# Performance work log

Hardware: AMD Instinct MI355X
Metric: run time of the kernel (lower is better)

The kernel has to match this reference:

```python
import jax, jax.numpy as jnp
import numpy as np

N = 50000
IN_DIM = 128
HID = 16
HEADS = 8
NUM_CLASSES = 16
NEG_SLOPE = 0.2


def _glorot(key, shape):
    fan_in, fan_out = shape[0], shape[-1]
    lim = float(np.sqrt(6.0 / (fan_in + fan_out)))
    return jax.random.uniform(key, shape, jnp.float32, -lim, lim)


def setup_inputs() -> dict:
    key = jax.random.key(0)
    ks = jax.random.split(key, 12)
    x = jax.random.normal(ks[0], (N, IN_DIM), jnp.float32)
    edge_index = jax.random.randint(ks[1], (2, 1600000), 0, N, jnp.int64)
    # conv1: in=IN_DIM, out per head=HID, heads=HEADS
    Wl1 = _glorot(ks[2], (IN_DIM, HEADS * HID))
    Wr1 = _glorot(ks[3], (IN_DIM, HEADS * HID))
    att1 = _glorot(ks[4], (HEADS, HID))
    b1 = jnp.zeros((HEADS * HID,), jnp.float32)
    # conv2: in=HID*HEADS, out per head=NUM_CLASSES
    Wl2 = _glorot(ks[5], (HEADS * HID, HEADS * NUM_CLASSES))
    Wr2 = _glorot(ks[6], (HEADS * HID, HEADS * NUM_CLASSES))
    att2 = _glorot(ks[7], (HEADS, NUM_CLASSES))
    b2 = jnp.zeros((HEADS * NUM_CLASSES,), jnp.float32)
    # final linear: NUM_CLASSES*HEADS -> NUM_CLASSES
    Wlin = _glorot(ks[8], (HEADS * NUM_CLASSES, NUM_CLASSES))
    blin = jnp.zeros((NUM_CLASSES,), jnp.float32)
    return dict(x=x, edge_index=edge_index, Wl1=Wl1, Wr1=Wr1, att1=att1, b1=b1,
                Wl2=Wl2, Wr2=Wr2, att2=att2, b2=b2, Wlin=Wlin, blin=blin)


def _gatv2_conv(x, src, dst, Wl, Wr, att, bias, heads, out_ch):
    n = x.shape[0]
    xl = (x @ Wl).reshape(n, heads, out_ch)  # source transform
    xr = (x @ Wr).reshape(n, heads, out_ch)  # target transform
    # additive attention logits per edge (GATv2)
    e = jax.nn.leaky_relu(xl[src] + xr[dst], NEG_SLOPE)          # [E,H,C]
    logits = jnp.einsum('ehc,hc->eh', e, att)                     # [E,H]
    # per-destination segment softmax
    m = jax.ops.segment_max(logits, dst, num_segments=n)          # [N,H]
    a = jnp.exp(logits - m[dst])                                  # [E,H]
    s = jax.ops.segment_sum(a, dst, num_segments=n)               # [N,H]
    alpha = a / (s[dst] + 1e-16)
    out = jax.ops.segment_sum(alpha[:, :, None] * xl[src], dst, num_segments=n)
    return out.reshape(n, heads * out_ch) + bias


def reference(x, edge_index, Wl1, Wr1, att1, b1, Wl2, Wr2, att2, b2, Wlin, blin):
    n = x.shape[0]
    # add self-loops (PyG GATv2Conv default add_self_loops=True)
    loop = jnp.arange(n, dtype=edge_index.dtype)
    src = jnp.concatenate([edge_index[0], loop])
    dst = jnp.concatenate([edge_index[1], loop])
    h = _gatv2_conv(x, src, dst, Wl1, Wr1, att1, b1, HEADS, HID)
    h = jax.nn.relu(h)  # dropout identity in eval mode
    h = _gatv2_conv(h, src, dst, Wl2, Wr2, att2, b2, HEADS, NUM_CLASSES)
    h = jax.nn.relu(h)
    logits = h @ Wlin + blin
    return jax.nn.log_softmax(logits, axis=1)
```

## Files before the change

kernel.cpp:

```cpp
#include <hip/hip_runtime.h>

#define HEADS 8
#define FDIM 128
#define NCLS 16
#define NEG_SLOPE 0.2f
#define LOG2E 1.4426950408889634f

typedef __attribute__((ext_vector_type(8))) short bf16x8;
typedef __attribute__((ext_vector_type(4))) float f32x4;

__device__ __forceinline__ unsigned short f2bf(float f) {
    unsigned u = __float_as_uint(f);
    unsigned r = u + 0x7FFFu + ((u >> 16) & 1u);
    return (unsigned short)(r >> 16);
}

__global__ __launch_bounds__(256) void gemm_csr(const float* __restrict__ Xf,
                                                const unsigned short* __restrict__ Xb,
                                                const float* __restrict__ W0,
                                                const float* __restrict__ W1,
                                                unsigned short* __restrict__ Y0,
                                                unsigned short* __restrict__ Y1,
                                                int n,
                                                const int* __restrict__ srcs,
                                                const int* __restrict__ dsts,
                                                int* __restrict__ cnt,
                                                int* __restrict__ adj,
                                                int E0, int pad, int GB, int SB) {
    __shared__ __align__(16) unsigned short ws[8 * 4 * 64 * 8];
    const int t = threadIdx.x;
    const int x = blockIdx.x;
    int gIdx;
    if (SB > 0) {
        if ((x % 5) == 4) {
            int i = (x / 5) * 256 + t;
            const int stride = SB * 256;
            for (; i < E0; i += stride) {
                const int d = dsts[i];
                const int rk = atomicAdd(&cnt[d], 1);
                if (rk < pad) adj[(size_t)d * pad + rk] = srcs[i];
            }
            return;
        }
        gIdx = (x / 5) * 4 + (x % 5);
    } else {
        gIdx = x;
    }
    const int side = (gIdx >= GB) ? 1 : 0;
    const float* W = side ? W1 : W0;
    unsigned short* Y = side ? Y1 : Y0;
    const int bid = side ? gIdx - GB : gIdx;

#pragma unroll
    for (int i = 0; i < 16; i++) {
        const int f = t + i * 256;
        const int k = f >> 5, n4 = f & 31;
        const float4 v = *(const float4*)(W + k * 128 + n4 * 4);
        const int kc = k >> 5, q = (k >> 3) & 3, j = k & 7;
        const float vv[4] = {v.x, v.y, v.z, v.w};
#pragma unroll
        for (int e = 0; e < 4; e++) {
            const int nn = n4 * 4 + e;
            ws[((((nn >> 4) * 4 + kc) * 64 + q * 16 + (nn & 15)) << 3) + j] = f2bf(vv[e]);
        }
    }
    __syncthreads();

    const int w = t >> 6, lane = t & 63;
    const int q = lane >> 4, m = lane & 15;
    const bf16x8* wb = (const bf16x8*)ws;
    const int Gh = (n + 63) >> 6;

    for (int tile = bid; tile < Gh; tile += GB) {
        const int nb = tile * 64;
        const int arow = nb + w * 16 + m;
        bf16x8 af[4];
        if (arow < n) {
            if (Xb) {
                const unsigned short* xp = Xb + (size_t)arow * 128 + q * 8;
#pragma unroll
                for (int kc = 0; kc < 4; kc++) af[kc] = *(const bf16x8*)(xp + kc * 32);
            } else {
                const float* xp = Xf + (size_t)arow * 128 + q * 8;
#pragma unroll
                for (int kc = 0; kc < 4; kc++) {
                    const float4 v0 = *(const float4*)(xp + kc * 32);
                    const float4 v1 = *(const float4*)(xp + kc * 32 + 4);
                    union { unsigned short us[8]; bf16x8 b; } pk;
                    pk.us[0] = f2bf(v0.x); pk.us[1] = f2bf(v0.y);
                    pk.us[2] = f2bf(v0.z); pk.us[3] = f2bf(v0.w);
                    pk.us[4] = f2bf(v1.x); pk.us[5] = f2bf(v1.y);
                    pk.us[6] = f2bf(v1.z); pk.us[7] = f2bf(v1.w);
                    af[kc] = pk.b;
                }
            }
        } else {
#pragma unroll
            for (int kc = 0; kc < 4; kc++) af[kc] = (bf16x8){0,0,0,0,0,0,0,0};
        }
        f32x4 acc[8];
#pragma unroll
        for (int i = 0; i < 8; i++) acc[i] = (f32x4){0.f, 0.f, 0.f, 0.f};
#pragma unroll
        for (int kc = 0; kc < 4; kc++) {
#pragma unroll
            for (int ct = 0; ct < 8; ct++)
                acc[ct] = __builtin_amdgcn_mfma_f32_16x16x32_bf16(
                    af[kc], wb[(ct * 4 + kc) * 64 + lane], acc[ct], 0, 0, 0);
        }
#pragma unroll
        for (int ct = 0; ct < 8; ct++) {
#pragma unroll
            for (int r = 0; r < 4; r++) {
                const int row = nb + w * 16 + q * 4 + r;
                if (row < n) Y[(size_t)row * 128 + ct * 16 + m] = f2bf(acc[ct][r]);
            }
        }
    }
}

#define GATHER_EDGE4(SRC, GATE)                                              \
    {                                                                        \
        const uint4 lv_ = *(const uint4*)(xl + (size_t)(SRC) * FDIM + col);  \
        const float l0_ = __uint_as_float(lv_.x << 16);                      \
        const float l1_ = __uint_as_float(lv_.x & 0xFFFF0000u);              \
        const float l2_ = __uint_as_float(lv_.y << 16);                      \
        const float l3_ = __uint_as_float(lv_.y & 0xFFFF0000u);              \
        const float l4_ = __uint_as_float(lv_.z << 16);                      \
        const float l5_ = __uint_as_float(lv_.z & 0xFFFF0000u);              \
        const float l6_ = __uint_as_float(lv_.w << 16);                      \
        const float l7_ = __uint_as_float(lv_.w & 0xFFFF0000u);              \
        float z_, p_;                                                        \
        z_ = l0_ + r0; z_ = fmaxf(z_, NEG_SLOPE * z_); p_  = z_ * a0;        \
        z_ = l1_ + r1; z_ = fmaxf(z_, NEG_SLOPE * z_); p_ += z_ * a1;        \
        z_ = l2_ + r2; z_ = fmaxf(z_, NEG_SLOPE * z_); p_ += z_ * a2;        \
        z_ = l3_ + r3; z_ = fmaxf(z_, NEG_SLOPE * z_); p_ += z_ * a3;        \
        z_ = l4_ + r4; z_ = fmaxf(z_, NEG_SLOPE * z_); p_ += z_ * a4;        \
        z_ = l5_ + r5; z_ = fmaxf(z_, NEG_SLOPE * z_); p_ += z_ * a5;        \
        z_ = l6_ + r6; z_ = fmaxf(z_, NEG_SLOPE * z_); p_ += z_ * a6;        \
        z_ = l7_ + r7; z_ = fmaxf(z_, NEG_SLOPE * z_); p_ += z_ * a7;        \
        p_ += __shfl_xor(p_, 1, 64);                                         \
        const float e_ = exp2f(p_ - mx) * (GATE);                            \
        s += e_;                                                             \
        c0 += e_ * l0_; c1 += e_ * l1_; c2 += e_ * l2_; c3 += e_ * l3_;      \
        c4 += e_ * l4_; c5 += e_ * l5_; c6 += e_ * l6_; c7 += e_ * l7_;      \
    }

template <bool HEAD>
__global__ __launch_bounds__(256) void node_gather(const unsigned short* __restrict__ xl,
                                                   const unsigned short* __restrict__ xr,
                                                   const float* __restrict__ att,
                                                   const int* __restrict__ adj,
                                                   const int* __restrict__ cnt,
                                                   const float* __restrict__ bias,
                                                   unsigned short* __restrict__ outC,
                                                   const float* __restrict__ headW,
                                                   const float* __restrict__ headB,
                                                   float* __restrict__ outH,
                                                   int n, int pad) {
    __shared__ float WsL[HEAD ? FDIM * NCLS : 1];
    __shared__ __align__(16) float stage[HEAD ? 4 : 1][FDIM];
    const int t = threadIdx.x;
    if (HEAD) {
        for (int i = t; i < FDIM * NCLS; i += 256) WsL[i] = headW[i];
        __syncthreads();
    }
    const int lane = t & 63;
    const int w = t >> 6;
    const int node = blockIdx.x * 4 + w;
    if (node >= n) return;
    const int g = lane >> 4;
    const int sub = lane & 15;
    const int col = sub * 8;
    float a0, a1, a2, a3, a4, a5, a6, a7;
    {
        const float4 v0 = *(const float4*)(att + col);
        const float4 v1 = *(const float4*)(att + col + 4);
        a0 = v0.x * LOG2E; a1 = v0.y * LOG2E; a2 = v0.z * LOG2E; a3 = v0.w * LOG2E;
        a4 = v1.x * LOG2E; a5 = v1.y * LOG2E; a6 = v1.z * LOG2E; a7 = v1.w * LOG2E;
    }
    float r0, r1, r2, r3, r4, r5, r6, r7;
    float sl0, sl1, sl2, sl3, sl4, sl5, sl6, sl7;
    {
        const uint4 rv = *(const uint4*)(xr + (size_t)node * FDIM + col);
        r0 = __uint_as_float(rv.x << 16); r1 = __uint_as_float(rv.x & 0xFFFF0000u);
        r2 = __uint_as_float(rv.y << 16); r3 = __uint_as_float(rv.y & 0xFFFF0000u);
        r4 = __uint_as_float(rv.z << 16); r5 = __uint_as_float(rv.z & 0xFFFF0000u);
        r6 = __uint_as_float(rv.w << 16); r7 = __uint_as_float(rv.w & 0xFFFF0000u);
        const uint4 lv = *(const uint4*)(xl + (size_t)node * FDIM + col);
        sl0 = __uint_as_float(lv.x << 16); sl1 = __uint_as_float(lv.x & 0xFFFF0000u);
        sl2 = __uint_as_float(lv.y << 16); sl3 = __uint_as_float(lv.y & 0xFFFF0000u);
        sl4 = __uint_as_float(lv.z << 16); sl5 = __uint_as_float(lv.z & 0xFFFF0000u);
        sl6 = __uint_as_float(lv.w << 16); sl7 = __uint_as_float(lv.w & 0xFFFF0000u);
    }
    float mx;
    {
        float z, p;
        z = sl0 + r0; z = fmaxf(z, NEG_SLOPE * z); p  = z * a0;
        z = sl1 + r1; z = fmaxf(z, NEG_SLOPE * z); p += z * a1;
        z = sl2 + r2; z = fmaxf(z, NEG_SLOPE * z); p += z * a2;
        z = sl3 + r3; z = fmaxf(z, NEG_SLOPE * z); p += z * a3;
        z = sl4 + r4; z = fmaxf(z, NEG_SLOPE * z); p += z * a4;
        z = sl5 + r5; z = fmaxf(z, NEG_SLOPE * z); p += z * a5;
        z = sl6 + r6; z = fmaxf(z, NEG_SLOPE * z); p += z * a6;
        z = sl7 + r7; z = fmaxf(z, NEG_SLOPE * z); p += z * a7;
        p += __shfl_xor(p, 1, 64);
        mx = p;
    }
    float s, c0, c1, c2, c3, c4, c5, c6, c7;
    if (g == 0) { s = 1.f; c0 = sl0; c1 = sl1; c2 = sl2; c3 = sl3;
                  c4 = sl4; c5 = sl5; c6 = sl6; c7 = sl7; }
    else        { s = 0.f; c0 = c1 = c2 = c3 = c4 = c5 = c6 = c7 = 0.f; }

    const int* ap = adj + (size_t)node * pad;
    const int deg = min(cnt[node], pad);
    int j = 0;
    for (; j + 8 <= deg; j += 8) {
        const int e0 = ap[j + g];
        const int e1 = ap[j + 4 + g];
        GATHER_EDGE4(e0, 1.f)
        GATHER_EDGE4(e1, 1.f)
    }
    for (; j < deg; j += 4) {
        const int idx = j + g;
        const int e0 = (idx < deg) ? ap[idx] : ap[deg - 1];
        const float gate = (idx < deg) ? 1.f : 0.f;
        GATHER_EDGE4(e0, gate)
    }
    s  += __shfl_xor(s, 16, 64);  s  += __shfl_xor(s, 32, 64);
    c0 += __shfl_xor(c0, 16, 64); c0 += __shfl_xor(c0, 32, 64);
    c1 += __shfl_xor(c1, 16, 64); c1 += __shfl_xor(c1, 32, 64);
    c2 += __shfl_xor(c2, 16, 64); c2 += __shfl_xor(c2, 32, 64);
    c3 += __shfl_xor(c3, 16, 64); c3 += __shfl_xor(c3, 32, 64);
    c4 += __shfl_xor(c4, 16, 64); c4 += __shfl_xor(c4, 32, 64);
    c5 += __shfl_xor(c5, 16, 64); c5 += __shfl_xor(c5, 32, 64);
    c6 += __shfl_xor(c6, 16, 64); c6 += __shfl_xor(c6, 32, 64);
    c7 += __shfl_xor(c7, 16, 64); c7 += __shfl_xor(c7, 32, 64);

    const float inv = 1.f / (s + 1e-16f);
    float o0, o1, o2, o3, o4, o5, o6, o7;
    {
        const float4 b0 = *(const float4*)(bias + col);
        const float4 b1 = *(const float4*)(bias + col + 4);
        o0 = fmaxf(c0 * inv + b0.x, 0.f); o1 = fmaxf(c1 * inv + b0.y, 0.f);
        o2 = fmaxf(c2 * inv + b0.z, 0.f); o3 = fmaxf(c3 * inv + b0.w, 0.f);
        o4 = fmaxf(c4 * inv + b1.x, 0.f); o5 = fmaxf(c5 * inv + b1.y, 0.f);
        o6 = fmaxf(c6 * inv + b1.z, 0.f); o7 = fmaxf(c7 * inv + b1.w, 0.f);
    }

    if (!HEAD) {
        if (g == 0) {
            union { unsigned short us[8]; uint4 u4; } pk;
            pk.us[0] = f2bf(o0); pk.us[1] = f2bf(o1);
            pk.us[2] = f2bf(o2); pk.us[3] = f2bf(o3);
            pk.us[4] = f2bf(o4); pk.us[5] = f2bf(o5);
            pk.us[6] = f2bf(o6); pk.us[7] = f2bf(o7);
            *(uint4*)(outC + (size_t)node * FDIM + col) = pk.u4;
        }
        return;
    }
    if (g == 0) {
        *(float4*)&stage[w][col]     = make_float4(o0, o1, o2, o3);
        *(float4*)&stage[w][col + 4] = make_float4(o4, o5, o6, o7);
    }
    const int cls = lane & 15;
    const int q = lane >> 4;
    float acc = 0.f;
#pragma unroll
    for (int k = 0; k < 32; k++)
        acc += stage[w][q * 32 + k] * WsL[(q * 32 + k) * NCLS + cls];
    acc += __shfl_xor(acc, 16, 64);
    acc += __shfl_xor(acc, 32, 64);
    acc += headB[cls];
    float m2 = acc;
    m2 = fmaxf(m2, __shfl_xor(m2, 8, 64));
    m2 = fmaxf(m2, __shfl_xor(m2, 4, 64));
    m2 = fmaxf(m2, __shfl_xor(m2, 2, 64));
    m2 = fmaxf(m2, __shfl_xor(m2, 1, 64));
    float sm = __expf(acc - m2);
    sm += __shfl_xor(sm, 8, 64);
    sm += __shfl_xor(sm, 4, 64);
    sm += __shfl_xor(sm, 2, 64);
    sm += __shfl_xor(sm, 1, 64);
    if (lane < 16)
        outH[(size_t)node * NCLS + cls] = acc - m2 - __logf(sm);
}

extern "C" void kernel_launch(void* const* d_in, const int* in_sizes, int n_in,
                              void* d_out, int out_size, void* d_ws, size_t ws_size,
                              hipStream_t stream) {
    const float* x    = (const float*)d_in[0];
    const int*   edge = (const int*)d_in[1];
    const float* Wl1  = (const float*)d_in[2];
    const float* Wr1  = (const float*)d_in[3];
    const float* att1 = (const float*)d_in[4];
    const float* b1   = (const float*)d_in[5];
    const float* Wl2  = (const float*)d_in[6];
    const float* Wr2  = (const float*)d_in[7];
    const float* att2 = (const float*)d_in[8];
    const float* b2   = (const float*)d_in[9];
    const float* Wlin = (const float*)d_in[10];
    const float* blin = (const float*)d_in[11];

    const int N = in_sizes[0] / FDIM;
    const int E0 = in_sizes[1] / 2;
    const int* srcs = edge;
    const int* dsts = edge + E0;

    int PAD = 96;
    {
        size_t need = (size_t)3 * N * FDIM * 2 + (size_t)N * 4 + (size_t)N * PAD * 4;
        if (need > ws_size) PAD = 72;
    }

    unsigned short* A = (unsigned short*)d_ws;
    unsigned short* B = A + (size_t)N * FDIM;
    unsigned short* C = B + (size_t)N * FDIM;
    int* cnt   = (int*)(C + (size_t)N * FDIM);
    int* adj   = cnt + N;

    const int GB = 512;
    const int SB = 256;
    const int node_blocks = (N + 3) / 4;

    hipMemsetAsync(cnt, 0, (size_t)N * sizeof(int), stream);

    gemm_csr<<<5 * SB, 256, 0, stream>>>(
        x, nullptr, Wl1, Wr1, A, B, N, srcs, dsts, cnt, adj, E0, PAD, GB, SB);
    node_gather<false><<<node_blocks, 256, 0, stream>>>(
        A, B, att1, adj, cnt, b1, C, nullptr, nullptr, nullptr, N, PAD);

    gemm_csr<<<2 * GB, 256, 0, stream>>>(
        nullptr, C, Wl2, Wr2, A, B, N, nullptr, nullptr, nullptr, nullptr, 0, PAD, GB, 0);
    node_gather<true><<<node_blocks, 256, 0, stream>>>(
        A, B, att2, adj, cnt, b2, nullptr, Wlin, blin, (float*)d_out, N, PAD);
}
```

Measured before the change: 359.1 us.

## Compute transposed GEMM tiles of 128 rows per block with vectorized stores

The GEMM now processes 128 rows per block, two 16-row subtiles per wave. Each LDS weight fragment feeds two MFMAs, and the operands are swapped so the output is transposed, which lets each lane write 4 contiguous bf16 values with one 8-byte store instead of scalar 2-byte stores. The grid is now sized to cover N exactly with GB=ceil(N/128), and the edge-scatter blocks are interleaved 1-in-4 instead of 1-in-5. The trade-off is higher register pressure from two accumulator sets and fewer scatter blocks relative to GEMM blocks.

After: 423.9 us. 18.1% more time.

```diff
diff --git a/kernel.cpp b/kernel.cpp
--- a/kernel.cpp
+++ b/kernel.cpp
@@ -32,8 +32,8 @@
     const int x = blockIdx.x;
     int gIdx;
     if (SB > 0) {
-        if ((x % 5) == 4) {
-            int i = (x / 5) * 256 + t;
+        if ((x & 3) == 3) {
+            int i = (x >> 2) * 256 + t;
             const int stride = SB * 256;
             for (; i < E0; i += stride) {
                 const int d = dsts[i];
@@ -42,10 +42,11 @@
             }
             return;
         }
-        gIdx = (x / 5) * 4 + (x % 5);
+        gIdx = (x >> 2) * 3 + (x & 3);
     } else {
         gIdx = x;
     }
+    if (gIdx >= 2 * GB) return;
     const int side = (gIdx >= GB) ? 1 : 0;
     const float* W = side ? W1 : W0;
     unsigned short* Y = side ? Y1 : Y0;
@@ -67,21 +68,32 @@
     __syncthreads();
 
     const int w = t >> 6, lane = t & 63;
-    const int q = lane >> 4, m = lane & 15;
+    const int q = lane >> 4, jd = lane & 15;
     const bf16x8* wb = (const bf16x8*)ws;
-    const int Gh = (n + 63) >> 6;
-
-    for (int tile = bid; tile < Gh; tile += GB) {
-        const int nb = tile * 64;
-        const int arow = nb + w * 16 + m;
-        bf16x8 af[4];
-        if (arow < n) {
-            if (Xb) {
-                const unsigned short* xp = Xb + (size_t)arow * 128 + q * 8;
-#pragma unroll
-                for (int kc = 0; kc < 4; kc++) af[kc] = *(const bf16x8*)(xp + kc * 32);
-            } else {
-                const float* xp = Xf + (size_t)arow * 128 + q * 8;
+
+    for (int sb = bid * 128; sb < n; sb += GB * 128) {
+        const int row0 = sb + w * 32 + jd;
+        const int row1 = row0 + 16;
+        bf16x8 bx0[4], bx1[4];
+#pragma unroll
+        for (int kc = 0; kc < 4; kc++) {
+            bx0[kc] = (bf16x8){0,0,0,0,0,0,0,0};
+            bx1[kc] = (bf16x8){0,0,0,0,0,0,0,0};
+        }
+        if (Xb) {
+            if (row0 < n) {
+                const unsigned short* xp = Xb + (size_t)row0 * 128 + q * 8;
+#pragma unroll
+                for (int kc = 0; kc < 4; kc++) bx0[kc] = *(const bf16x8*)(xp + kc * 32);
+            }
+            if (row1 < n) {
+                const unsigned short* xp = Xb + (size_t)row1 * 128 + q * 8;
+#pragma unroll
+                for (int kc = 0; kc < 4; kc++) bx1[kc] = *(const bf16x8*)(xp + kc * 32);
+            }
+        } else {
+            if (row0 < n) {
+                const float* xp = Xf + (size_t)row0 * 128 + q * 8;
 #pragma unroll
                 for (int kc = 0; kc < 4; kc++) {
                     const float4 v0 = *(const float4*)(xp + kc * 32);
@@ -91,29 +103,57 @@
                     pk.us[2] = f2bf(v0.z); pk.us[3] = f2bf(v0.w);
                     pk.us[4] = f2bf(v1.x); pk.us[5] = f2bf(v1.y);
                     pk.us[6] = f2bf(v1.z); pk.us[7] = f2bf(v1.w);
-                    af[kc] = pk.b;
+                    bx0[kc] = pk.b;
                 }
             }
-        } else {
-#pragma unroll
-            for (int kc = 0; kc < 4; kc++) af[kc] = (bf16x8){0,0,0,0,0,0,0,0};
-        }
-        f32x4 acc[8];
-#pragma unroll
-        for (int i = 0; i < 8; i++) acc[i] = (f32x4){0.f, 0.f, 0.f, 0.f};
+            if (row1 < n) {
+                const float* xp = Xf + (size_t)row1 * 128 + q * 8;
+#pragma unroll
+                for (int kc = 0; kc < 4; kc++) {
+                    const float4 v0 = *(const float4*)(xp + kc * 32);
+                    const float4 v1 = *(const float4*)(xp + kc * 32 + 4);
+                    union { unsigned short us[8]; bf16x8 b; } pk;
+                    pk.us[0] = f2bf(v0.x); pk.us[1] = f2bf(v0.y);
+                    pk.us[2] = f2bf(v0.z); pk.us[3] = f2bf(v0.w);
+                    pk.us[4] = f2bf(v1.x); pk.us[5] = f2bf(v1.y);
+                    pk.us[6] = f2bf(v1.z); pk.us[7] = f2bf(v1.w);
+                    bx1[kc] = pk.b;
+                }
+            }
+        }
+        f32x4 acc0[8], acc1[8];
+#pragma unroll
+        for (int i = 0; i < 8; i++) {
+            acc0[i] = (f32x4){0.f, 0.f, 0.f, 0.f};
+            acc1[i] = (f32x4){0.f, 0.f, 0.f, 0.f};
+        }
 #pragma unroll
         for (int kc = 0; kc < 4; kc++) {
 #pragma unroll
-            for (int ct = 0; ct < 8; ct++)
-                acc[ct] = __builtin_amdgcn_mfma_f32_16x16x32_bf16(
-                    af[kc], wb[(ct * 4 + kc) * 64 + lane], acc[ct], 0, 0, 0);
-        }
-#pragma unroll
-        for (int ct = 0; ct < 8; ct++) {
-#pragma unroll
-            for (int r = 0; r < 4; r++) {
-                const int row = nb + w * 16 + q * 4 + r;
-                if (row < n) Y[(size_t)row * 128 + ct * 16 + m] = f2bf(acc[ct][r]);
+            for (int ct = 0; ct < 8; ct++) {
+                const bf16x8 aw = wb[(ct * 4 + kc) * 64 + lane];
+                acc0[ct] = __builtin_amdgcn_mfma_f32_16x16x32_bf16(aw, bx0[kc], acc0[ct], 0, 0, 0);
+                acc1[ct] = __builtin_amdgcn_mfma_f32_16x16x32_bf16(aw, bx1[kc], acc1[ct], 0, 0, 0);
+            }
+        }
+        if (row0 < n) {
+            unsigned short* yp = Y + (size_t)row0 * 128 + q * 4;
+#pragma unroll
+            for (int ct = 0; ct < 8; ct++) {
+                union { unsigned short us[4]; uint2 u2; } pk;
+                pk.us[0] = f2bf(acc0[ct][0]); pk.us[1] = f2bf(acc0[ct][1]);
+                pk.us[2] = f2bf(acc0[ct][2]); pk.us[3] = f2bf(acc0[ct][3]);
+                *(uint2*)(yp + ct * 16) = pk.u2;
+            }
+        }
+        if (row1 < n) {
+            unsigned short* yp = Y + (size_t)row1 * 128 + q * 4;
+#pragma unroll
+            for (int ct = 0; ct < 8; ct++) {
+                union { unsigned short us[4]; uint2 u2; } pk;
+                pk.us[0] = f2bf(acc1[ct][0]); pk.us[1] = f2bf(acc1[ct][1]);
+                pk.us[2] = f2bf(acc1[ct][2]); pk.us[3] = f2bf(acc1[ct][3]);
+                *(uint2*)(yp + ct * 16) = pk.u2;
             }
         }
     }
@@ -319,18 +359,19 @@
     int* cnt   = (int*)(C + (size_t)N * FDIM);
     int* adj   = cnt + N;
 
-    const int GB = 512;
-    const int SB = 256;
+    const int GB = (N + 127) / 128;
+    const int G  = 2 * GB;
+    const int SB = (G + 2) / 3;
     const int node_blocks = (N + 3) / 4;
 
     hipMemsetAsync(cnt, 0, (size_t)N * sizeof(int), stream);
 
-    gemm_csr<<<5 * SB, 256, 0, stream>>>(
+    gemm_csr<<<4 * SB, 256, 0, stream>>>(
         x, nullptr, Wl1, Wr1, A, B, N, srcs, dsts, cnt, adj, E0, PAD, GB, SB);
     node_gather<false><<<node_blocks, 256, 0, stream>>>(
         A, B, att1, adj, cnt, b1, C, nullptr, nullptr, nullptr, N, PAD);
 
-    gemm_csr<<<2 * GB, 256, 0, stream>>>(
+    gemm_csr<<<G, 256, 0, stream>>>(
         nullptr, C, Wl2, Wr2, A, B, N, nullptr, nullptr, nullptr, nullptr, 0, PAD, GB, 0);
     node_gather<true><<<node_blocks, 256, 0, stream>>>(
         A, B, att2, adj, cnt, b2, nullptr, Wlin, blin, (float*)d_out, N, PAD);
```

## Use one tile per GEMM block, swap MFMA operands, and stage output through LDS

Applied to the files above, without the earlier changes.

The GEMM+CSR kernel now gives each block a single 64-row tile instead of a grid-stride loop, with grid sizes derived from N. The MFMA operands are swapped so each lane holds four consecutive output columns for one row. Results are packed into an LDS tile and written back as coalesced 16-byte row stores, replacing scattered 2-byte stores. This adds LDS usage and more blocks, each of which reloads and converts the weight matrix into shared memory, and it also rescales the CSR-building edge blocks.

New measurement: 365.5 us. About the same (+1.8%).

```diff
diff --git a/kernel.cpp b/kernel.cpp
--- a/kernel.cpp
+++ b/kernel.cpp
@@ -28,6 +28,7 @@
                                                 int* __restrict__ adj,
                                                 int E0, int pad, int GB, int SB) {
     __shared__ __align__(16) unsigned short ws[8 * 4 * 64 * 8];
+    __shared__ __align__(16) unsigned short ys[64 * 132];
     const int t = threadIdx.x;
     const int x = blockIdx.x;
     int gIdx;
@@ -46,10 +47,11 @@
     } else {
         gIdx = x;
     }
+    if (gIdx >= 2 * GB) return;
     const int side = (gIdx >= GB) ? 1 : 0;
     const float* W = side ? W1 : W0;
     unsigned short* Y = side ? Y1 : Y0;
-    const int bid = side ? gIdx - GB : gIdx;
+    const int nb = (side ? gIdx - GB : gIdx) * 64;
 
 #pragma unroll
     for (int i = 0; i < 16; i++) {
@@ -67,54 +69,63 @@
     __syncthreads();
 
     const int w = t >> 6, lane = t & 63;
-    const int q = lane >> 4, m = lane & 15;
+    const int q = lane >> 4, jd = lane & 15;
     const bf16x8* wb = (const bf16x8*)ws;
-    const int Gh = (n + 63) >> 6;
-
-    for (int tile = bid; tile < Gh; tile += GB) {
-        const int nb = tile * 64;
-        const int arow = nb + w * 16 + m;
-        bf16x8 af[4];
-        if (arow < n) {
-            if (Xb) {
-                const unsigned short* xp = Xb + (size_t)arow * 128 + q * 8;
-#pragma unroll
-                for (int kc = 0; kc < 4; kc++) af[kc] = *(const bf16x8*)(xp + kc * 32);
-            } else {
-                const float* xp = Xf + (size_t)arow * 128 + q * 8;
-#pragma unroll
-                for (int kc = 0; kc < 4; kc++) {
-                    const float4 v0 = *(const float4*)(xp + kc * 32);
-                    const float4 v1 = *(const float4*)(xp + kc * 32 + 4);
-                    union { unsigned short us[8]; bf16x8 b; } pk;
-                    pk.us[0] = f2bf(v0.x); pk.us[1] = f2bf(v0.y);
-                    pk.us[2] = f2bf(v0.z); pk.us[3] = f2bf(v0.w);
-                    pk.us[4] = f2bf(v1.x); pk.us[5] = f2bf(v1.y);
-                    pk.us[6] = f2bf(v1.z); pk.us[7] = f2bf(v1.w);
-                    af[kc] = pk.b;
-                }
+
+    const int row = nb + w * 16 + jd;
+    bf16x8 bx[4];
+#pragma unroll
+    for (int kc = 0; kc < 4; kc++) bx[kc] = (bf16x8){0,0,0,0,0,0,0,0};
+    if (row < n) {
+        if (Xb) {
+            const unsigned short* xp = Xb + (size_t)row * 128 + q * 8;
+#pragma unroll
+            for (int kc = 0; kc < 4; kc++) bx[kc] = *(const bf16x8*)(xp + kc * 32);
+        } else {
+            const float* xp = Xf + (size_t)row * 128 + q * 8;
+#pragma unroll
+            for (int kc = 0; kc < 4; kc++) {
+                const float4 v0 = *(const float4*)(xp + kc * 32);
+                const float4 v1 = *(const float4*)(xp + kc * 32 + 4);
+                union { unsigned short us[8]; bf16x8 b; } pk;
+                pk.us[0] = f2bf(v0.x); pk.us[1] = f2bf(v0.y);
+                pk.us[2] = f2bf(v0.z); pk.us[3] = f2bf(v0.w);
+                pk.us[4] = f2bf(v1.x); pk.us[5] = f2bf(v1.y);
+                pk.us[6] = f2bf(v1.z); pk.us[7] = f2bf(v1.w);
+                bx[kc] = pk.b;
             }
-        } else {
-#pragma unroll
-            for (int kc = 0; kc < 4; kc++) af[kc] = (bf16x8){0,0,0,0,0,0,0,0};
-        }
-        f32x4 acc[8];
-#pragma unroll
-        for (int i = 0; i < 8; i++) acc[i] = (f32x4){0.f, 0.f, 0.f, 0.f};
-#pragma unroll
-        for (int kc = 0; kc < 4; kc++) {
-#pragma unroll
-            for (int ct = 0; ct < 8; ct++)
-                acc[ct] = __builtin_amdgcn_mfma_f32_16x16x32_bf16(
-                    af[kc], wb[(ct * 4 + kc) * 64 + lane], acc[ct], 0, 0, 0);
-        }
+        }
+    }
+    f32x4 acc[8];
+#pragma unroll
+    for (int i = 0; i < 8; i++) acc[i] = (f32x4){0.f, 0.f, 0.f, 0.f};
+#pragma unroll
+    for (int kc = 0; kc < 4; kc++) {
+#pragma unroll
+        for (int ct = 0; ct < 8; ct++)
+            acc[ct] = __builtin_amdgcn_mfma_f32_16x16x32_bf16(
+                wb[(ct * 4 + kc) * 64 + lane], bx[kc], acc[ct], 0, 0, 0);
+    }
+    {
+        unsigned short* yrow = ys + (w * 16 + jd) * 132;
 #pragma unroll
         for (int ct = 0; ct < 8; ct++) {
-#pragma unroll
-            for (int r = 0; r < 4; r++) {
-                const int row = nb + w * 16 + q * 4 + r;
-                if (row < n) Y[(size_t)row * 128 + ct * 16 + m] = f2bf(acc[ct][r]);
-            }
+            union { unsigned short us[4]; uint2 u2; } pk;
+            pk.us[0] = f2bf(acc[ct][0]); pk.us[1] = f2bf(acc[ct][1]);
+            pk.us[2] = f2bf(acc[ct][2]); pk.us[3] = f2bf(acc[ct][3]);
+            *(uint2*)(yrow + ct * 16 + q * 4) = pk.u2;
+        }
+    }
+    {
+        const int rr = lane >> 4;
+        const int ch = lane & 15;
+#pragma unroll
+        for (int i = 0; i < 4; i++) {
+            const int lrow = w * 16 + i * 4 + rr;
+            const int grow = nb + lrow;
+            const uint4 v = *(const uint4*)(ys + lrow * 132 + ch * 8);
+            if (grow < n)
+                *(uint4*)(Y + (size_t)grow * 128 + ch * 8) = v;
         }
     }
 }
@@ -319,8 +330,9 @@
     int* cnt   = (int*)(C + (size_t)N * FDIM);
     int* adj   = cnt + N;
 
-    const int GB = 512;
-    const int SB = 256;
+    const int GB = (N + 63) / 64;
+    const int G  = 2 * GB;
+    const int SB = (G + 3) / 4;
     const int node_blocks = (N + 3) / 4;
 
     hipMemsetAsync(cnt, 0, (size_t)N * sizeof(int), stream);
@@ -330,7 +342,7 @@
     node_gather<false><<<node_blocks, 256, 0, stream>>>(
         A, B, att1, adj, cnt, b1, C, nullptr, nullptr, nullptr, N, PAD);
 
-    gemm_csr<<<2 * GB, 256, 0, stream>>>(
+    gemm_csr<<<G, 256, 0, stream>>>(
         nullptr, C, Wl2, Wr2, A, B, N, nullptr, nullptr, nullptr, nullptr, 0, PAD, GB, 0);
     node_gather<true><<<node_blocks, 256, 0, stream>>>(
         A, B, att2, adj, cnt, b2, nullptr, Wlin, blin, (float*)d_out, N, PAD);
```
